# Optimization experiments

Measured on AMD Instinct MI355X. Metric: run time of the kernel, lower is better.

The kernel has to match this reference:

```python
import jax, jax.numpy as jnp
import numpy as np

B = 128          # graphs
NPG = 512        # nodes per graph
N = B * NPG      # total nodes
DEG = 8
E = N * DEG      # total edges (intra-graph)
D = 100          # num_feature_dim / num_node_labels
HID = 128        # config.hidden
HEADS = 8
F1 = 20          # per-head dim of first GATConv in each GATNet
RATIO = 0.5
K = int(np.ceil(RATIO * NPG))  # nodes kept per graph by SAGPooling
NEG_SLOPE = 0.2


def setup_inputs() -> dict:
    key = jax.random.key(0)
    ks = jax.random.split(key, 24)
    x = jax.random.randint(ks[0], (N,), 0, D)
    # intra-graph random edges: local ids in [0, NPG) + graph offset
    src_l = jax.random.randint(ks[1], (B, NPG * DEG), 0, NPG)
    dst_l = jax.random.randint(ks[2], (B, NPG * DEG), 0, NPG)
    off = (jnp.arange(B) * NPG)[:, None]
    edge_index = jnp.stack([(src_l + off).ravel(), (dst_l + off).ravel()])
    batch = jnp.repeat(jnp.arange(B), NPG)

    def lin(k, fan_in, fan_out):
        return jax.random.normal(k, (fan_in, fan_out), jnp.float32) / np.sqrt(fan_in)

    def att(k, h, f):
        return jax.random.normal(k, (h, f), jnp.float32) * 0.1

    p = {
        # GATNet A (conv1): GATConv(D, 20, heads=8) then GATConv(160, HID, heads=1)
        "W_a1": lin(ks[3], D, HEADS * F1), "asrc_a1": att(ks[4], HEADS, F1),
        "adst_a1": att(ks[5], HEADS, F1), "b_a1": jnp.zeros((HEADS * F1,), jnp.float32),
        "W_a2": lin(ks[6], HEADS * F1, HID), "asrc_a2": att(ks[7], 1, HID),
        "adst_a2": att(ks[8], 1, HID), "b_a2": jnp.zeros((HID,), jnp.float32),
        # GATNet B (conv4): GATConv(HID, 20, heads=8) then GATConv(160, HID, heads=1)
        "W_b1": lin(ks[9], HID, HEADS * F1), "asrc_b1": att(ks[10], HEADS, F1),
        "adst_b1": att(ks[11], HEADS, F1), "b_b1": jnp.zeros((HEADS * F1,), jnp.float32),
        "W_b2": lin(ks[12], HEADS * F1, HID), "asrc_b2": att(ks[13], 1, HID),
        "adst_b2": att(ks[14], 1, HID), "b_b2": jnp.zeros((HID,), jnp.float32),
        # SAGPooling GraphConv(HID, 1)
        "w_rel": lin(ks[15], HID, 1), "w_root": lin(ks[16], HID, 1),
        "b_pool": jnp.zeros((1,), jnp.float32),
    }
    return {"x": x, "edge_index": edge_index, "batch": batch, **p}


def _gat_conv(h, src, dst, W, asrc, adst, b):
    """PyG GATConv (with self-loops already included in src/dst)."""
    Hh, Ff = asrc.shape
    z = (h @ W).reshape(N, Hh, Ff)                       # [N,H,F]
    es = jnp.sum(z * asrc, axis=-1)                      # [N,H] source logits
    ed = jnp.sum(z * adst, axis=-1)                      # [N,H] dest logits
    e = jax.nn.leaky_relu(es[src] + ed[dst], NEG_SLOPE)  # [E',H]
    m = jax.ops.segment_max(e, dst, num_segments=N)
    m = jnp.where(jnp.isfinite(m), m, 0.0)
    ex = jnp.exp(e - m[dst])
    den = jax.ops.segment_sum(ex, dst, num_segments=N)
    alpha = ex / (den[dst] + 1e-16)
    out = jax.ops.segment_sum(z[src] * alpha[:, :, None], dst, num_segments=N)
    return out.reshape(N, Hh * Ff) + b


def reference(x, edge_index, batch,
              W_a1, asrc_a1, adst_a1, b_a1, W_a2, asrc_a2, adst_a2, b_a2,
              W_b1, asrc_b1, adst_b1, b_b1, W_b2, asrc_b2, adst_b2, b_b2,
              w_rel, w_root, b_pool):
    src, dst = edge_index[0], edge_index[1]
    loops = jnp.arange(N)
    src_sl = jnp.concatenate([src, loops])  # GATConv adds self loops
    dst_sl = jnp.concatenate([dst, loops])

    h = jax.nn.one_hot(x, D, dtype=jnp.float32)
    # GATNet A: conv1 -> relu -> conv2 ; outer relu (dropout is eval no-op)
    h = jax.nn.relu(_gat_conv(h, src_sl, dst_sl, W_a1, asrc_a1, adst_a1, b_a1))
    h = _gat_conv(h, src_sl, dst_sl, W_a2, asrc_a2, adst_a2, b_a2)
    h = jax.nn.relu(h)
    # GATNet B
    h = jax.nn.relu(_gat_conv(h, src_sl, dst_sl, W_b1, asrc_b1, adst_b1, b_b1))
    h = _gat_conv(h, src_sl, dst_sl, W_b2, asrc_b2, adst_b2, b_b2)
    h = jax.nn.relu(h)

    # SAGPooling: GraphConv(HID,1) score (no self loops), tanh, per-graph top-k
    nbr = jax.ops.segment_sum(h[src], dst, num_segments=N)
    score = jnp.tanh(nbr @ w_rel + h @ w_root + b_pool).ravel()   # [N]
    sv, si = jax.lax.top_k(score.reshape(B, NPG), K)              # [B,K]
    perm = (si + (jnp.arange(B) * NPG)[:, None]).ravel()          # global node ids
    x_sel = h[perm] * sv.ravel()[:, None]                         # [B*K, HID]
    pooled = jnp.max(x_sel.reshape(B, K, HID), axis=1)            # global_max_pool
    batch_out = jnp.repeat(jnp.arange(B), K)
    return (pooled, perm, sv.ravel(), batch_out)
```

## Files before the change

kernel.cpp:

```cpp
#include <hip/hip_runtime.h>
#include <math.h>

#define N_NODES 65536
#define NPG     512
#define NGRAPH  128
#define E_EDGES 524288
#define MAXDEG  64
#define NHEADS  8
#define F1      20
#define HID     128
#define D160    160
#define KSEL    256

typedef unsigned short ushort_t;
typedef unsigned int   uint_t;
typedef unsigned long long u64;
typedef __attribute__((ext_vector_type(8))) short short8;
typedef __attribute__((ext_vector_type(4))) float f32x4;

__device__ __forceinline__ float lrelu(float x){ return x > 0.f ? x : 0.2f*x; }
__device__ __forceinline__ ushort_t f2bf(float f){
    uint_t u = __float_as_uint(f);
    return (ushort_t)((u + 0x7FFFu + ((u >> 16) & 1u)) >> 16);
}
__device__ __forceinline__ float bf2f(ushort_t u){ return __uint_as_float(((uint_t)u) << 16); }
__device__ __forceinline__ float bflo(uint_t v){ return __uint_as_float(v << 16); }
__device__ __forceinline__ float bfhi(uint_t v){ return __uint_as_float(v & 0xFFFF0000u); }
__device__ __forceinline__ int xswz(int bid, int nblocks){
    return (bid & 7) * (nblocks >> 3) + (bid >> 3);
}
__device__ __forceinline__ float rdlanef(float v, int i){
    return __uint_as_float((uint_t)__builtin_amdgcn_readlane(__float_as_int(v), i));
}

__device__ __forceinline__ u64 comp_make(float s, int idx){
    uint_t u = __float_as_uint(s);
    u ^= (u & 0x80000000u) ? 0xFFFFFFFFu : 0x80000000u;
    return ((u64)u << 32) | (u64)(511 - idx);
}
__device__ __forceinline__ float comp_score(u64 c){
    uint_t u = (uint_t)(c >> 32);
    u ^= (u & 0x80000000u) ? 0x80000000u : 0xFFFFFFFFu;
    return __uint_as_float(u);
}
__device__ __forceinline__ int comp_idx(u64 c){ return 511 - (int)(c & 0x1FFu); }
__device__ __forceinline__ u64 shfl_xor_u64(u64 x, int m){
    uint_t lo = __shfl_xor((uint_t)x, m);
    uint_t hi = __shfl_xor((uint_t)(x >> 32), m);
    return ((u64)hi << 32) | lo;
}

__global__ void k_zero(uint4* __restrict__ p){
    p[blockIdx.x*blockDim.x + threadIdx.x] = (uint4){0,0,0,0};
}

__global__ void k_build_ell(const int* __restrict__ src, const int* __restrict__ dst,
                            int* __restrict__ deg, int* __restrict__ ell){
    int blk = xswz(blockIdx.x, E_EDGES/256);
    int e = blk*blockDim.x + threadIdx.x;
    int d = dst[e];
    int p = atomicAdd(&deg[d], 1);
    if(p < MAXDEG) ell[d*MAXDEG + p] = src[e];
}

__global__ void k_a1_z(const int* __restrict__ x, const float* __restrict__ W,
                       const float* __restrict__ asrc, const float* __restrict__ adst,
                       ushort_t* __restrict__ z8, float* __restrict__ es8, float* __restrict__ ed8){
    int blk = xswz(blockIdx.x, N_NODES*NHEADS/256);
    int t = blk*blockDim.x + threadIdx.x;
    int n = t >> 3, h = t & 7;
    int lbl = x[n];
    const float* wrow = W + lbl*D160 + h*F1;
    const float* as = asrc + h*F1;
    const float* ad = adst + h*F1;
    uint_t* zr = (uint_t*)(z8 + (size_t)n*D160 + h*F1);
    float es = 0.f, ed = 0.f;
    #pragma unroll
    for(int f=0; f<10; ++f){
        float v0 = wrow[2*f], v1 = wrow[2*f+1];
        zr[f] = (uint_t)f2bf(v0) | ((uint_t)f2bf(v1) << 16);
        es += v0*as[2*f] + v1*as[2*f+1];
        ed += v0*ad[2*f] + v1*ad[2*f+1];
    }
    es8[t] = es; ed8[t] = ed;
}

__global__ void k_attn8(const int* __restrict__ deg, const int* __restrict__ ell,
                        const ushort_t* __restrict__ z8, const float* __restrict__ es8,
                        const float* __restrict__ ed8, const float* __restrict__ bias,
                        ushort_t* __restrict__ out){
    int blk = xswz(blockIdx.x, N_NODES*NHEADS/256);
    int t = blk*blockDim.x + threadIdx.x;
    int n = t >> 3, h = t & 7;
    int dg = deg[n]; if(dg > MAXDEG) dg = MAXDEG;
    float edn = ed8[t];
    float eself = lrelu(es8[t] + edn);
    const int* el = ell + n*MAXDEG;
    float m = eself;
    {
        int i = 0;
        for(; i+2 <= dg; i += 2){
            int sa = el[i], sb = el[i+1];
            float ea = es8[sa*NHEADS + h], eb = es8[sb*NHEADS + h];
            m = fmaxf(m, fmaxf(lrelu(ea + edn), lrelu(eb + edn)));
        }
        if(i < dg){
            float ea = es8[el[i]*NHEADS + h];
            m = fmaxf(m, lrelu(ea + edn));
        }
    }
    float w = expf(eself - m);
    float den = w;
    float acc[F1];
    const uint_t* zn = (const uint_t*)(z8 + (size_t)n*D160 + h*F1);
    #pragma unroll
    for(int f=0; f<10; ++f){
        uint_t v = zn[f];
        acc[2*f]   = w*bflo(v);
        acc[2*f+1] = w*bfhi(v);
    }
    {
        int i = 0;
        for(; i+2 <= dg; i += 2){
            int sa = el[i], sb = el[i+1];
            float ea = es8[sa*NHEADS + h], eb = es8[sb*NHEADS + h];
            const uint_t* za = (const uint_t*)(z8 + (size_t)sa*D160 + h*F1);
            const uint_t* zb = (const uint_t*)(z8 + (size_t)sb*D160 + h*F1);
            float wa = expf(lrelu(ea + edn) - m);
            float wb = expf(lrelu(eb + edn) - m);
            den += wa + wb;
            #pragma unroll
            for(int f=0; f<10; ++f){
                uint_t va = za[f], vb = zb[f];
                acc[2*f]   += wa*bflo(va) + wb*bflo(vb);
                acc[2*f+1] += wa*bfhi(va) + wb*bfhi(vb);
            }
        }
        if(i < dg){
            int sa = el[i];
            float ea = es8[sa*NHEADS + h];
            const uint_t* za = (const uint_t*)(z8 + (size_t)sa*D160 + h*F1);
            float wa = expf(lrelu(ea + edn) - m);
            den += wa;
            #pragma unroll
            for(int f=0; f<10; ++f){
                uint_t va = za[f];
                acc[2*f]   += wa*bflo(va);
                acc[2*f+1] += wa*bfhi(va);
            }
        }
    }
    float inv = 1.f/(den + 1e-16f);
    uint_t* o = (uint_t*)(out + (size_t)n*D160 + h*F1);
    const float* bb = bias + h*F1;
    #pragma unroll
    for(int f=0; f<10; ++f){
        float v0 = fmaxf(acc[2*f]*inv   + bb[2*f],   0.f);
        float v1 = fmaxf(acc[2*f+1]*inv + bb[2*f+1], 0.f);
        o[f] = (uint_t)f2bf(v0) | ((uint_t)f2bf(v1) << 16);
    }
}

template<int IN, int OUT, bool DOT>
__global__ __launch_bounds__(256) void k_gemm_mfma(const ushort_t* __restrict__ A,
                                                   const float* __restrict__ W,
                                                   ushort_t* __restrict__ C,
                                                   const float* __restrict__ va,
                                                   const float* __restrict__ vb,
                                                   float* __restrict__ oa,
                                                   float* __restrict__ ob){
    constexpr int NT = OUT/16;
    constexpr int KS = IN/32;
    constexpr int LDW = IN + 8;
    __shared__ __align__(16) ushort_t Wt[OUT*LDW];
    int tid = threadIdx.x;
    for(int i = tid; i < IN*OUT; i += 256){
        int k = i / OUT, n = i - k*OUT;
        Wt[n*LDW + k] = f2bf(W[i]);
    }
    __syncthreads();
    int blk = xswz(blockIdx.x, N_NODES/64);
    int wave = tid >> 6, lane = tid & 63;
    int col16 = lane & 15;
    int kq = (lane >> 4) * 8;
    int row = blk*64 + wave*16 + col16;
    const ushort_t* Ar = A + (size_t)row*IN + kq;
    f32x4 acc[NT];
    #pragma unroll
    for(int c=0;c<NT;++c) acc[c] = (f32x4){0.f,0.f,0.f,0.f};
    #pragma unroll
    for(int ks=0; ks<KS; ++ks){
        short8 af = *reinterpret_cast<const short8*>(Ar + ks*32);
        #pragma unroll
        for(int c=0;c<NT;++c){
            short8 bf = *reinterpret_cast<const short8*>(&Wt[(c*16 + col16)*LDW + ks*32 + kq]);
            acc[c] = __builtin_amdgcn_mfma_f32_16x16x32_bf16(af, bf, acc[c], 0, 0, 0);
        }
    }
    int rbase = blk*64 + wave*16 + (lane >> 4)*4;
    #pragma unroll
    for(int c=0;c<NT;++c){
        #pragma unroll
        for(int r=0;r<4;++r){
            C[(size_t)(rbase + r)*OUT + c*16 + col16] = f2bf(acc[c][r]);
        }
    }
    if(DOT){
        float pa[4] = {0,0,0,0}, pb[4] = {0,0,0,0};
        #pragma unroll
        for(int c=0;c<NT;++c){
            float a = va[c*16 + col16];
            float b = vb[c*16 + col16];
            #pragma unroll
            for(int r=0;r<4;++r){ pa[r] += acc[c][r]*a; pb[r] += acc[c][r]*b; }
        }
        #pragma unroll
        for(int o=1;o<16;o<<=1){
            #pragma unroll
            for(int r=0;r<4;++r){ pa[r] += __shfl_xor(pa[r], o); pb[r] += __shfl_xor(pb[r], o); }
        }
        if(col16 == 0){
            #pragma unroll
            for(int r=0;r<4;++r){ oa[rbase + r] = pa[r]; ob[rbase + r] = pb[r]; }
        }
    }
}

__global__ __launch_bounds__(256) void k_gemm_b1(const ushort_t* __restrict__ A,
                                                 const float* __restrict__ W,
                                                 const float* __restrict__ asrc,
                                                 const float* __restrict__ adst,
                                                 ushort_t* __restrict__ C,
                                                 float* __restrict__ es8,
                                                 float* __restrict__ ed8){
    constexpr int IN = HID, OUTW = D160, NT = 11, KS = IN/32, LDW = IN + 8;
    __shared__ __align__(16) ushort_t Wt[(OUTW+16)*LDW];
    int tid = threadIdx.x;
    for(int i = tid; i < IN*OUTW; i += 256){
        int k = i / OUTW, n = i - k*OUTW;
        Wt[n*LDW + k] = f2bf(W[i]);
    }
    for(int i = tid; i < IN*16; i += 256){
        int k = i >> 4, j = i & 15;
        const float* av = (j < 8 ? asrc : adst) + (j & 7)*F1;
        const float* wr = W + k*OUTW + (j & 7)*F1;
        float s = 0.f;
        #pragma unroll
        for(int f=0; f<F1; ++f) s += wr[f]*av[f];
        Wt[(OUTW + j)*LDW + k] = f2bf(s);
    }
    __syncthreads();
    int blk = xswz(blockIdx.x, N_NODES/64);
    int wave = tid >> 6, lane = tid & 63;
    int col16 = lane & 15;
    int kq = (lane >> 4) * 8;
    int row = blk*64 + wave*16 + col16;
    const ushort_t* Ar = A + (size_t)row*IN + kq;
    f32x4 acc[NT];
    #pragma unroll
    for(int c=0;c<NT;++c) acc[c] = (f32x4){0.f,0.f,0.f,0.f};
    #pragma unroll
    for(int ks=0; ks<KS; ++ks){
        short8 af = *reinterpret_cast<const short8*>(Ar + ks*32);
        #pragma unroll
        for(int c=0;c<NT;++c){
            short8 bf = *reinterpret_cast<const short8*>(&Wt[(c*16 + col16)*LDW + ks*32 + kq]);
            acc[c] = __builtin_amdgcn_mfma_f32_16x16x32_bf16(af, bf, acc[c], 0, 0, 0);
        }
    }
    int rbase = blk*64 + wave*16 + (lane >> 4)*4;
    #pragma unroll
    for(int c=0;c<10;++c){
        #pragma unroll
        for(int r=0;r<4;++r){
            C[(size_t)(rbase + r)*OUTW + c*16 + col16] = f2bf(acc[c][r]);
        }
    }
    #pragma unroll
    for(int r=0;r<4;++r){
        float v = acc[10][r];
        if(col16 < 8) es8[(size_t)(rbase + r)*8 + col16] = v;
        else          ed8[(size_t)(rbase + r)*8 + (col16 - 8)] = v;
    }
}

template<typename OutT, bool DOT>
__global__ void k_attn1(const int* __restrict__ deg, const int* __restrict__ ell,
                        const ushort_t* __restrict__ Z, const float* __restrict__ es,
                        const float* __restrict__ ed, const float* __restrict__ bias,
                        OutT* __restrict__ out,
                        const float* __restrict__ wa, const float* __restrict__ wb,
                        float* __restrict__ oa, float* __restrict__ ob){
    int blk = xswz(blockIdx.x, N_NODES/4);
    int gt = blk*blockDim.x + threadIdx.x;
    int n = gt >> 6;
    int l = threadIdx.x & 63;
    int dg = deg[n]; if(dg > MAXDEG) dg = MAXDEG;
    float edn = ed[n];
    float eself = lrelu(es[n] + edn);
    int s_l = 0; float e_l = -1e30f;
    if(l < dg){ s_l = ell[n*MAXDEG + l]; e_l = lrelu(es[s_l] + edn); }
    float m = fmaxf(e_l, eself);
    for(int o=32;o>0;o>>=1) m = fmaxf(m, __shfl_xor(m,o));
    float w_l = (l < dg) ? expf(e_l - m) : 0.f;
    float den = w_l;
    for(int o=32;o>0;o>>=1) den += __shfl_xor(den,o);
    float wself = expf(eself - m);
    den += wself;
    const uint_t* Zu = (const uint_t*)Z;
    uint_t zn = Zu[(size_t)n*64 + l];
    float acc0 = wself*bflo(zn);
    float acc1 = wself*bfhi(zn);
    int i = 0;
    for(; i+4 <= dg; i += 4){
        int s0 = __builtin_amdgcn_readlane(s_l, i);
        int s1 = __builtin_amdgcn_readlane(s_l, i+1);
        int s2 = __builtin_amdgcn_readlane(s_l, i+2);
        int s3 = __builtin_amdgcn_readlane(s_l, i+3);
        uint_t z0 = Zu[(size_t)s0*64 + l];
        uint_t z1 = Zu[(size_t)s1*64 + l];
        uint_t z2 = Zu[(size_t)s2*64 + l];
        uint_t z3 = Zu[(size_t)s3*64 + l];
        float w0 = rdlanef(w_l, i);
        float w1 = rdlanef(w_l, i+1);
        float w2 = rdlanef(w_l, i+2);
        float w3 = rdlanef(w_l, i+3);
        acc0 += w0*bflo(z0) + w1*bflo(z1);
        acc1 += w0*bfhi(z0) + w1*bfhi(z1);
        acc0 += w2*bflo(z2) + w3*bflo(z3);
        acc1 += w2*bfhi(z2) + w3*bfhi(z3);
    }
    for(; i < dg; ++i){
        int s0 = __builtin_amdgcn_readlane(s_l, i);
        float w0 = rdlanef(w_l, i);
        uint_t z0 = Zu[(size_t)s0*64 + l];
        acc0 += w0*bflo(z0);
        acc1 += w0*bfhi(z0);
    }
    float inv = 1.f/(den + 1e-16f);
    float2 bb = ((const float2*)bias)[l];
    float r0 = fmaxf(acc0*inv + bb.x, 0.f);
    float r1 = fmaxf(acc1*inv + bb.y, 0.f);
    if(sizeof(OutT) == 2){
        ((uint_t*)out)[(size_t)n*64 + l] = (uint_t)f2bf(r0) | ((uint_t)f2bf(r1) << 16);
    } else {
        float2 rv; rv.x = r0; rv.y = r1;
        ((float2*)out)[(size_t)n*64 + l] = rv;
    }
    if(DOT){
        float2 a2 = ((const float2*)wa)[l];
        float2 b2 = ((const float2*)wb)[l];
        float pa = r0*a2.x + r1*a2.y;
        float pb = r0*b2.x + r1*b2.y;
        for(int o=32;o>0;o>>=1){ pa += __shfl_xor(pa,o); pb += __shfl_xor(pb,o); }
        if(l==0){ oa[n] = pa; ob[n] = pb; }
    }
}

__global__ void k_score(const int* __restrict__ deg, const int* __restrict__ ell,
                        const float* __restrict__ yrel, const float* __restrict__ rroot,
                        const float* __restrict__ bpool, float* __restrict__ score){
    int blk = xswz(blockIdx.x, N_NODES/256);
    int n = blk*blockDim.x + threadIdx.x;
    int dg = deg[n]; if(dg > MAXDEG) dg = MAXDEG;
    float s = rroot[n] + bpool[0];
    const int* el = ell + n*MAXDEG;
    int i = 0;
    for(; i+4 <= dg; i += 4){
        float y0 = yrel[el[i]],   y1 = yrel[el[i+1]];
        float y2 = yrel[el[i+2]], y3 = yrel[el[i+3]];
        s += (y0 + y1) + (y2 + y3);
    }
    for(; i < dg; ++i) s += yrel[el[i]];
    score[n] = tanhf(s);
}

__global__ __launch_bounds__(512) void k_topk_pool(const float* __restrict__ score,
                                                   const float* __restrict__ H,
                                                   float* __restrict__ pooled,
                                                   float* __restrict__ perm_f,
                                                   float* __restrict__ sv,
                                                   float* __restrict__ batch_f){
    __shared__ int   sidx[KSEL];
    __shared__ float sval[KSEL];
    __shared__ float pmax[512];
    int g = xswz(blockIdx.x, NGRAPH);
    int base = g*NPG;
    int t = threadIdx.x;
    if(t < 64){
        int l = t;
        u64 v[8];
        #pragma unroll
        for(int r=0;r<8;++r){
            int i = r*64 + l;
            v[r] = comp_make(score[base + i], i);
        }
        #pragma unroll
        for(int kk=1; kk<=9; ++kk){
            int k = 1 << kk;
            #pragma unroll
            for(int jj=kk-1; jj>=0; --jj){
                int j = 1 << jj;
                if(j < 64){
                    bool lower = (l & j) == 0;
                    #pragma unroll
                    for(int r=0;r<8;++r){
                        int i = r*64 + l;
                        u64 p = shfl_xor_u64(v[r], j);
                        bool desc = (i & k) == 0;
                        u64 mx = v[r] > p ? v[r] : p;
                        u64 mn = v[r] > p ? p : v[r];
                        v[r] = (lower == desc) ? mx : mn;
                    }
                } else {
                    int jr = j >> 6;
                    #pragma unroll
                    for(int r=0;r<8;++r){
                        if((r & jr) == 0){
                            int rp = r | jr;
                            int i = r*64 + l;
                            bool desc = (i & k) == 0;
                            u64 a = v[r], b = v[rp];
                            u64 mx = a > b ? a : b;
                            u64 mn = a > b ? b : a;
                            v[r]  = desc ? mx : mn;
                            v[rp] = desc ? mn : mx;
                        }
                    }
                }
            }
        }
        #pragma unroll
        for(int r=0;r<4;++r){
            int i = r*64 + l;
            int idx = comp_idx(v[r]);
            float s = comp_score(v[r]);
            perm_f[g*KSEL + i]  = (float)(base + idx);
            sv[g*KSEL + i]      = s;
            batch_f[g*KSEL + i] = (float)g;
            sidx[i] = idx; sval[i] = s;
        }
    }
    __syncthreads();
    int c = t & 127, kc = t >> 7;
    float mx = -1e30f;
    for(int kk = kc*64; kk < kc*64 + 64; ++kk){
        mx = fmaxf(mx, H[(size_t)(base + sidx[kk])*HID + c] * sval[kk]);
    }
    pmax[t] = mx;
    __syncthreads();
    if(t < HID){
        pooled[g*HID + t] = fmaxf(fmaxf(pmax[t], pmax[t+128]),
                                  fmaxf(pmax[t+256], pmax[t+384]));
    }
}

extern "C" void kernel_launch(void* const* d_in, const int* in_sizes, int n_in,
                              void* d_out, int out_size, void* d_ws, size_t ws_size,
                              hipStream_t stream) {
    const int*   x       = (const int*)  d_in[0];
    const int*   eidx    = (const int*)  d_in[1];
    const float* W_a1    = (const float*)d_in[3];
    const float* asrc_a1 = (const float*)d_in[4];
    const float* adst_a1 = (const float*)d_in[5];
    const float* b_a1    = (const float*)d_in[6];
    const float* W_a2    = (const float*)d_in[7];
    const float* asrc_a2 = (const float*)d_in[8];
    const float* adst_a2 = (const float*)d_in[9];
    const float* b_a2    = (const float*)d_in[10];
    const float* W_b1    = (const float*)d_in[11];
    const float* asrc_b1 = (const float*)d_in[12];
    const float* adst_b1 = (const float*)d_in[13];
    const float* b_b1    = (const float*)d_in[14];
    const float* W_b2    = (const float*)d_in[15];
    const float* asrc_b2 = (const float*)d_in[16];
    const float* adst_b2 = (const float*)d_in[17];
    const float* b_b2    = (const float*)d_in[18];
    const float* w_rel   = (const float*)d_in[19];
    const float* w_root  = (const float*)d_in[20];
    const float* b_pool  = (const float*)d_in[21];

    const int* e_src = eidx;
    const int* e_dst = eidx + E_EDGES;

    char* ws = (char*)d_ws;
    size_t off = 0;
    auto alloc = [&](size_t bytes)->char*{
        char* p = ws + off;
        off += (bytes + 255) & ~(size_t)255;
        return p;
    };
    int*      deg   = (int*)     alloc((size_t)N_NODES*4);
    int*      ell   = (int*)     alloc((size_t)N_NODES*MAXDEG*4);
    ushort_t* z8    = (ushort_t*)alloc((size_t)N_NODES*D160*2);
    ushort_t* h8    = (ushort_t*)alloc((size_t)N_NODES*D160*2);
    ushort_t* zc    = (ushort_t*)alloc((size_t)N_NODES*HID*2);
    ushort_t* hmid  = (ushort_t*)alloc((size_t)N_NODES*HID*2);
    float*    hfin  = (float*)   alloc((size_t)N_NODES*HID*4);
    float*    es8   = (float*)   alloc((size_t)N_NODES*NHEADS*4);
    float*    ed8   = (float*)   alloc((size_t)N_NODES*NHEADS*4);
    float*    es1   = (float*)   alloc((size_t)N_NODES*4);
    float*    ed1   = (float*)   alloc((size_t)N_NODES*4);
    float*    yrel  = (float*)   alloc((size_t)N_NODES*4);
    float*    rroot = (float*)   alloc((size_t)N_NODES*4);
    float*    score = (float*)   alloc((size_t)N_NODES*4);
    (void)ws_size; (void)n_in; (void)in_sizes; (void)out_size;

    float* out      = (float*)d_out;
    float* pooled   = out;
    float* perm_f   = out + NGRAPH*HID;
    float* sv       = perm_f + NGRAPH*KSEL;
    float* batch_f  = sv + NGRAPH*KSEL;

    k_zero<<<N_NODES*4/(16*256), 256, 0, stream>>>((uint4*)deg);
    k_build_ell<<<E_EDGES/256, 256, 0, stream>>>(e_src, e_dst, deg, ell);

    k_a1_z<<<N_NODES*NHEADS/256, 256, 0, stream>>>(x, W_a1, asrc_a1, adst_a1, z8, es8, ed8);
    k_attn8<<<N_NODES*NHEADS/256, 256, 0, stream>>>(deg, ell, z8, es8, ed8, b_a1, h8);

    k_gemm_mfma<D160, HID, true><<<N_NODES/64, 256, 0, stream>>>(h8, W_a2, zc, asrc_a2, adst_a2, es1, ed1);
    k_attn1<ushort_t, false><<<N_NODES/4, 256, 0, stream>>>(deg, ell, zc, es1, ed1, b_a2, hmid,
                                                            nullptr, nullptr, nullptr, nullptr);

    k_gemm_b1<<<N_NODES/64, 256, 0, stream>>>(hmid, W_b1, asrc_b1, adst_b1, z8, es8, ed8);
    k_attn8<<<N_NODES*NHEADS/256, 256, 0, stream>>>(deg, ell, z8, es8, ed8, b_b1, h8);

    k_gemm_mfma<D160, HID, true><<<N_NODES/64, 256, 0, stream>>>(h8, W_b2, zc, asrc_b2, adst_b2, es1, ed1);
    k_attn1<float, true><<<N_NODES/4, 256, 0, stream>>>(deg, ell, zc, es1, ed1, b_b2, hfin,
                                                        w_rel, w_root, yrel, rroot);

    k_score<<<N_NODES/256, 256, 0, stream>>>(deg, ell, yrel, rroot, b_pool, score);
    k_topk_pool<<<NGRAPH, NPG, 0, stream>>>(score, hfin, pooled, perm_f, sv, batch_f);
}
```

Before: 256.6 us.

## Exploit one-hot input via per-label table, drop softmax max pass, bf16 final features

```diff
diff --git a/kernel.cpp b/kernel.cpp
--- a/kernel.cpp
+++ b/kernel.cpp
@@ -11,6 +11,7 @@
 #define HID     128
 #define D160    160
 #define KSEL    256
+#define NLBL    100
 
 typedef unsigned short ushort_t;
 typedef unsigned int   uint_t;
@@ -63,26 +64,94 @@
     if(p < MAXDEG) ell[d*MAXDEG + p] = src[e];
 }
 
-__global__ void k_a1_z(const int* __restrict__ x, const float* __restrict__ W,
-                       const float* __restrict__ asrc, const float* __restrict__ adst,
-                       ushort_t* __restrict__ z8, float* __restrict__ es8, float* __restrict__ ed8){
+__global__ void k_prep_a(const float* __restrict__ W, const float* __restrict__ asrc,
+                         const float* __restrict__ adst,
+                         ushort_t* __restrict__ Wbf, float* __restrict__ esT,
+                         float* __restrict__ edT){
+    int lbl = blockIdx.x;
+    int f = threadIdx.x;
+    const float* wrow = W + lbl*D160;
+    Wbf[lbl*D160 + f] = f2bf(wrow[f]);
+    if(f < 16){
+        int h = f & 7;
+        const float* av = ((f < 8) ? asrc : adst) + h*F1;
+        float s = 0.f;
+        #pragma unroll
+        for(int k=0; k<F1; ++k) s += wrow[h*F1 + k]*av[k];
+        if(f < 8) esT[lbl*8 + h] = s;
+        else      edT[lbl*8 + h] = s;
+    }
+}
+
+__global__ __launch_bounds__(256) void k_attn8_a(const int* __restrict__ x,
+        const int* __restrict__ deg, const int* __restrict__ ell,
+        const ushort_t* __restrict__ Wbf, const float* __restrict__ esT,
+        const float* __restrict__ edT, const float* __restrict__ bias,
+        ushort_t* __restrict__ out){
+    __shared__ __align__(16) ushort_t Wl[NLBL*D160];
+    __shared__ float esL[NLBL*8], edL[NLBL*8];
+    int tid = threadIdx.x;
+    for(int i = tid; i < NLBL*D160/8; i += 256)
+        ((uint4*)Wl)[i] = ((const uint4*)Wbf)[i];
+    for(int i = tid; i < NLBL*8; i += 256){ esL[i] = esT[i]; edL[i] = edT[i]; }
+    __syncthreads();
     int blk = xswz(blockIdx.x, N_NODES*NHEADS/256);
-    int t = blk*blockDim.x + threadIdx.x;
+    int t = blk*256 + tid;
     int n = t >> 3, h = t & 7;
+    int dg = deg[n]; if(dg > MAXDEG) dg = MAXDEG;
     int lbl = x[n];
-    const float* wrow = W + lbl*D160 + h*F1;
-    const float* as = asrc + h*F1;
-    const float* ad = adst + h*F1;
-    uint_t* zr = (uint_t*)(z8 + (size_t)n*D160 + h*F1);
-    float es = 0.f, ed = 0.f;
+    float edn = edL[lbl*8 + h];
+    float wself = expf(lrelu(esL[lbl*8 + h] + edn));
+    float den = wself;
+    float acc[F1];
+    {
+        const uint_t* zn = (const uint_t*)Wl + lbl*80 + h*10;
+        #pragma unroll
+        for(int f=0; f<10; ++f){
+            uint_t v = zn[f];
+            acc[2*f]   = wself*bflo(v);
+            acc[2*f+1] = wself*bfhi(v);
+        }
+    }
+    const int* el = ell + n*MAXDEG;
+    int i = 0;
+    for(; i+2 <= dg; i += 2){
+        int sa = el[i], sb = el[i+1];
+        int la = x[sa], lb = x[sb];
+        float wa = expf(lrelu(esL[la*8 + h] + edn));
+        float wb = expf(lrelu(esL[lb*8 + h] + edn));
+        den += wa + wb;
+        const uint_t* za = (const uint_t*)Wl + la*80 + h*10;
+        const uint_t* zb = (const uint_t*)Wl + lb*80 + h*10;
+        #pragma unroll
+        for(int f=0; f<10; ++f){
+            uint_t va = za[f], vb = zb[f];
+            acc[2*f]   += wa*bflo(va) + wb*bflo(vb);
+            acc[2*f+1] += wa*bfhi(va) + wb*bfhi(vb);
+        }
+    }
+    if(i < dg){
+        int sa = el[i];
+        int la = x[sa];
+        float wa = expf(lrelu(esL[la*8 + h] + edn));
+        den += wa;
+        const uint_t* za = (const uint_t*)Wl + la*80 + h*10;
+        #pragma unroll
+        for(int f=0; f<10; ++f){
+            uint_t va = za[f];
+            acc[2*f]   += wa*bflo(va);
+            acc[2*f+1] += wa*bfhi(va);
+        }
+    }
+    float inv = 1.f/(den + 1e-16f);
+    uint_t* o = (uint_t*)(out + (size_t)n*D160 + h*F1);
+    const float* bb = bias + h*F1;
     #pragma unroll
     for(int f=0; f<10; ++f){
-        float v0 = wrow[2*f], v1 = wrow[2*f+1];
-        zr[f] = (uint_t)f2bf(v0) | ((uint_t)f2bf(v1) << 16);
-        es += v0*as[2*f] + v1*as[2*f+1];
-        ed += v0*ad[2*f] + v1*ad[2*f+1];
-    }
-    es8[t] = es; ed8[t] = ed;
+        float v0 = fmaxf(acc[2*f]*inv   + bb[2*f],   0.f);
+        float v1 = fmaxf(acc[2*f+1]*inv + bb[2*f+1], 0.f);
+        o[f] = (uint_t)f2bf(v0) | ((uint_t)f2bf(v1) << 16);
+    }
 }
 
 __global__ void k_attn8(const int* __restrict__ deg, const int* __restrict__ ell,
@@ -94,60 +163,44 @@
     int n = t >> 3, h = t & 7;
     int dg = deg[n]; if(dg > MAXDEG) dg = MAXDEG;
     float edn = ed8[t];
-    float eself = lrelu(es8[t] + edn);
-    const int* el = ell + n*MAXDEG;
-    float m = eself;
-    {
-        int i = 0;
-        for(; i+2 <= dg; i += 2){
-            int sa = el[i], sb = el[i+1];
-            float ea = es8[sa*NHEADS + h], eb = es8[sb*NHEADS + h];
-            m = fmaxf(m, fmaxf(lrelu(ea + edn), lrelu(eb + edn)));
-        }
-        if(i < dg){
-            float ea = es8[el[i]*NHEADS + h];
-            m = fmaxf(m, lrelu(ea + edn));
-        }
-    }
-    float w = expf(eself - m);
-    float den = w;
+    float wself = expf(lrelu(es8[t] + edn));
+    float den = wself;
     float acc[F1];
     const uint_t* zn = (const uint_t*)(z8 + (size_t)n*D160 + h*F1);
     #pragma unroll
     for(int f=0; f<10; ++f){
         uint_t v = zn[f];
-        acc[2*f]   = w*bflo(v);
-        acc[2*f+1] = w*bfhi(v);
-    }
-    {
-        int i = 0;
-        for(; i+2 <= dg; i += 2){
-            int sa = el[i], sb = el[i+1];
-            float ea = es8[sa*NHEADS + h], eb = es8[sb*NHEADS + h];
-            const uint_t* za = (const uint_t*)(z8 + (size_t)sa*D160 + h*F1);
-            const uint_t* zb = (const uint_t*)(z8 + (size_t)sb*D160 + h*F1);
-            float wa = expf(lrelu(ea + edn) - m);
-            float wb = expf(lrelu(eb + edn) - m);
-            den += wa + wb;
-            #pragma unroll
-            for(int f=0; f<10; ++f){
-                uint_t va = za[f], vb = zb[f];
-                acc[2*f]   += wa*bflo(va) + wb*bflo(vb);
-                acc[2*f+1] += wa*bfhi(va) + wb*bfhi(vb);
-            }
-        }
-        if(i < dg){
-            int sa = el[i];
-            float ea = es8[sa*NHEADS + h];
-            const uint_t* za = (const uint_t*)(z8 + (size_t)sa*D160 + h*F1);
-            float wa = expf(lrelu(ea + edn) - m);
-            den += wa;
-            #pragma unroll
-            for(int f=0; f<10; ++f){
-                uint_t va = za[f];
-                acc[2*f]   += wa*bflo(va);
-                acc[2*f+1] += wa*bfhi(va);
-            }
+        acc[2*f]   = wself*bflo(v);
+        acc[2*f+1] = wself*bfhi(v);
+    }
+    const int* el = ell + n*MAXDEG;
+    int i = 0;
+    for(; i+2 <= dg; i += 2){
+        int sa = el[i], sb = el[i+1];
+        float ea = es8[sa*NHEADS + h], eb = es8[sb*NHEADS + h];
+        const uint_t* za = (const uint_t*)(z8 + (size_t)sa*D160 + h*F1);
+        const uint_t* zb = (const uint_t*)(z8 + (size_t)sb*D160 + h*F1);
+        float wa = expf(lrelu(ea + edn));
+        float wb = expf(lrelu(eb + edn));
+        den += wa + wb;
+        #pragma unroll
+        for(int f=0; f<10; ++f){
+            uint_t va = za[f], vb = zb[f];
+            acc[2*f]   += wa*bflo(va) + wb*bflo(vb);
+            acc[2*f+1] += wa*bfhi(va) + wb*bfhi(vb);
+        }
+    }
+    if(i < dg){
+        int sa = el[i];
+        float ea = es8[sa*NHEADS + h];
+        const uint_t* za = (const uint_t*)(z8 + (size_t)sa*D160 + h*F1);
+        float wa = expf(lrelu(ea + edn));
+        den += wa;
+        #pragma unroll
+        for(int f=0; f<10; ++f){
+            uint_t va = za[f];
+            acc[2*f]   += wa*bflo(va);
+            acc[2*f+1] += wa*bfhi(va);
         }
     }
     float inv = 1.f/(den + 1e-16f);
@@ -297,15 +350,11 @@
     int l = threadIdx.x & 63;
     int dg = deg[n]; if(dg > MAXDEG) dg = MAXDEG;
     float edn = ed[n];
-    float eself = lrelu(es[n] + edn);
-    int s_l = 0; float e_l = -1e30f;
-    if(l < dg){ s_l = ell[n*MAXDEG + l]; e_l = lrelu(es[s_l] + edn); }
-    float m = fmaxf(e_l, eself);
-    for(int o=32;o>0;o>>=1) m = fmaxf(m, __shfl_xor(m,o));
-    float w_l = (l < dg) ? expf(e_l - m) : 0.f;
+    float wself = expf(lrelu(es[n] + edn));
+    int s_l = 0; float w_l = 0.f;
+    if(l < dg){ s_l = ell[n*MAXDEG + l]; w_l = expf(lrelu(es[s_l] + edn)); }
     float den = w_l;
     for(int o=32;o>0;o>>=1) den += __shfl_xor(den,o);
-    float wself = expf(eself - m);
     den += wself;
     const uint_t* Zu = (const uint_t*)Z;
     uint_t zn = Zu[(size_t)n*64 + l];
@@ -376,7 +425,7 @@
 }
 
 __global__ __launch_bounds__(512) void k_topk_pool(const float* __restrict__ score,
-                                                   const float* __restrict__ H,
+                                                   const ushort_t* __restrict__ H,
                                                    float* __restrict__ pooled,
                                                    float* __restrict__ perm_f,
                                                    float* __restrict__ sv,
@@ -445,7 +494,7 @@
     int c = t & 127, kc = t >> 7;
     float mx = -1e30f;
     for(int kk = kc*64; kk < kc*64 + 64; ++kk){
-        mx = fmaxf(mx, H[(size_t)(base + sidx[kk])*HID + c] * sval[kk]);
+        mx = fmaxf(mx, bf2f(H[(size_t)(base + sidx[kk])*HID + c]) * sval[kk]);
     }
     pmax[t] = mx;
     __syncthreads();
@@ -496,7 +545,7 @@
     ushort_t* h8    = (ushort_t*)alloc((size_t)N_NODES*D160*2);
     ushort_t* zc    = (ushort_t*)alloc((size_t)N_NODES*HID*2);
     ushort_t* hmid  = (ushort_t*)alloc((size_t)N_NODES*HID*2);
-    float*    hfin  = (float*)   alloc((size_t)N_NODES*HID*4);
+    ushort_t* hfin  = (ushort_t*)alloc((size_t)N_NODES*HID*2);
     float*    es8   = (float*)   alloc((size_t)N_NODES*NHEADS*4);
     float*    ed8   = (float*)   alloc((size_t)N_NODES*NHEADS*4);
     float*    es1   = (float*)   alloc((size_t)N_NODES*4);
@@ -504,6 +553,9 @@
     float*    yrel  = (float*)   alloc((size_t)N_NODES*4);
     float*    rroot = (float*)   alloc((size_t)N_NODES*4);
     float*    score = (float*)   alloc((size_t)N_NODES*4);
+    ushort_t* Wbf   = (ushort_t*)alloc((size_t)NLBL*D160*2);
+    float*    esT   = (float*)   alloc((size_t)NLBL*8*4);
+    float*    edT   = (float*)   alloc((size_t)NLBL*8*4);
     (void)ws_size; (void)n_in; (void)in_sizes; (void)out_size;
 
     float* out      = (float*)d_out;
@@ -515,8 +567,8 @@
     k_zero<<<N_NODES*4/(16*256), 256, 0, stream>>>((uint4*)deg);
     k_build_ell<<<E_EDGES/256, 256, 0, stream>>>(e_src, e_dst, deg, ell);
 
-    k_a1_z<<<N_NODES*NHEADS/256, 256, 0, stream>>>(x, W_a1, asrc_a1, adst_a1, z8, es8, ed8);
-    k_attn8<<<N_NODES*NHEADS/256, 256, 0, stream>>>(deg, ell, z8, es8, ed8, b_a1, h8);
+    k_prep_a<<<NLBL, D160, 0, stream>>>(W_a1, asrc_a1, adst_a1, Wbf, esT, edT);
+    k_attn8_a<<<N_NODES*NHEADS/256, 256, 0, stream>>>(x, deg, ell, Wbf, esT, edT, b_a1, h8);
 
     k_gemm_mfma<D160, HID, true><<<N_NODES/64, 256, 0, stream>>>(h8, W_a2, zc, asrc_a2, adst_a2, es1, ed1);
     k_attn1<ushort_t, false><<<N_NODES/4, 256, 0, stream>>>(deg, ell, zc, es1, ed1, b_a2, hmid,
@@ -526,8 +578,8 @@
     k_attn8<<<N_NODES*NHEADS/256, 256, 0, stream>>>(deg, ell, z8, es8, ed8, b_b1, h8);
 
     k_gemm_mfma<D160, HID, true><<<N_NODES/64, 256, 0, stream>>>(h8, W_b2, zc, asrc_b2, adst_b2, es1, ed1);
-    k_attn1<float, true><<<N_NODES/4, 256, 0, stream>>>(deg, ell, zc, es1, ed1, b_b2, hfin,
-                                                        w_rel, w_root, yrel, rroot);
+    k_attn1<ushort_t, true><<<N_NODES/4, 256, 0, stream>>>(deg, ell, zc, es1, ed1, b_b2, hfin,
+                                                           w_rel, w_root, yrel, rroot);
 
     k_score<<<N_NODES/256, 256, 0, stream>>>(deg, ell, yrel, rroot, b_pool, score);
     k_topk_pool<<<NGRAPH, NPG, 0, stream>>>(score, hfin, pooled, perm_f, sv, batch_f);
```

Result: faster. 240.5 us (-6.3%).
